# Kernel tuning notes

Hardware: AMD Instinct MI355X
Metric: run time of the kernel (lower is better)

Reference implementation:

```python
import jax, jax.numpy as jnp
import numpy as np

B, R, N, D, H = 32, 5, 1024, 256, 256

def setup_inputs() -> dict:
    key = jax.random.key(0)
    k1, k2, k3, k4 = jax.random.split(key, 4)
    nodes = jax.random.normal(k1, (B, N, D), dtype=jnp.float32)
    adj = jax.random.uniform(k2, (B, R, N, N), dtype=jnp.float32)
    # kaiming_normal_ approximation: std = sqrt(2 / fan_in)
    std = np.sqrt(2.0 / D).astype(np.float32)
    w_0 = jax.random.normal(k3, (H, D), dtype=jnp.float32) * std
    w_r = jax.random.normal(k4, (R, H, D), dtype=jnp.float32) * std
    return {"nodes": nodes, "adj": adj, "w_0": w_0, "w_r": w_r}

def reference(nodes, adj, w_0, w_r):
    # nodes: (B,N,D), adj: (B,R,N,N), w_0: (H,D), w_r: (R,H,D)
    xw_0 = jnp.einsum('bnd,hd->bnh', nodes, w_0)            # (B,N,H)
    xw_r = jnp.einsum('bnd,rhd->brnh', nodes, w_r)          # (B,R,N,H)
    c_r = jnp.sum(adj, axis=-1, keepdims=True)              # (B,R,N,1)
    c_r = jnp.where(c_r == 0, jnp.ones_like(c_r), c_r)
    out = jnp.sum(xw_r / c_r, axis=1) + xw_0                # (B,N,H)
    # dropout is identity in eval mode
    return out
```

## Files before the change

### kernel.cpp

```cpp
#include <hip/hip_runtime.h>
#include <hip/hip_bf16.h>


#define BB 32
#define RR 5
#define NN 1024
#define DD 256
#define HH 256
#define MM (BB * NN)

typedef __attribute__((ext_vector_type(8))) short short8;
typedef __attribute__((ext_vector_type(4))) float f32x4;

__device__ __forceinline__ unsigned short f2bf(float f) {
    unsigned int u = __float_as_uint(f);
    unsigned int r = (u + 0x7FFFu + ((u >> 16) & 1u)) >> 16;
    return (unsigned short)r;
}

__global__ void cvt_kernel(const float* __restrict__ in,
                           unsigned short* __restrict__ out, int n) {
    int i = (blockIdx.x * blockDim.x + threadIdx.x) * 4;
    if (i >= n) return;
    float4 v = *reinterpret_cast<const float4*>(in + i);
    ushort4 o;
    o.x = f2bf(v.x); o.y = f2bf(v.y); o.z = f2bf(v.z); o.w = f2bf(v.w);
    *reinterpret_cast<ushort4*>(out + i) = o;
}

__global__ __launch_bounds__(256) void rowsum_kernel(const float* __restrict__ adj,
                                                     float* __restrict__ inv_c) {
    const int wave = blockIdx.x * 4 + (threadIdx.x >> 6);
    const int lane = threadIdx.x & 63;
    const float4* row4 = reinterpret_cast<const float4*>(adj + (size_t)wave * NN);
    float s = 0.f;
#pragma unroll
    for (int i = 0; i < 4; ++i) {
        float4 v = row4[lane + 64 * i];
        s += (v.x + v.y) + (v.z + v.w);
    }
#pragma unroll
    for (int off = 32; off > 0; off >>= 1) s += __shfl_down(s, off, 64);
    if (lane == 0) {
        float c = (s == 0.f) ? 1.f : s;
        inv_c[wave] = 1.f / c;
    }
}

__global__ __launch_bounds__(256) void gemm_kernel(
    const unsigned short* __restrict__ nodesb,
    const unsigned short* __restrict__ wb,
    const float* __restrict__ inv_c,
    float* __restrict__ out) {
    const int lane = threadIdx.x & 63;
    const int wv   = threadIdx.x >> 6;
    const int row_base = blockIdx.x * 64;
    const int col_base = blockIdx.y * 64 + wv * 16;
    const int m    = lane & 15;
    const int quad = lane >> 4;
    const int kofs = quad * 8;

    f32x4 acc[6][4];
#pragma unroll
    for (int s = 0; s < 6; ++s)
#pragma unroll
        for (int t = 0; t < 4; ++t) acc[s][t] = (f32x4){0.f, 0.f, 0.f, 0.f};

    const unsigned short* aptr = nodesb + (size_t)(row_base + m) * DD + kofs;
    const unsigned short* bptr = wb + (size_t)(col_base + m) * DD + kofs;

#pragma unroll
    for (int k = 0; k < DD; k += 32) {
        short8 afr[4];
#pragma unroll
        for (int t = 0; t < 4; ++t)
            afr[t] = *reinterpret_cast<const short8*>(aptr + (size_t)t * 16 * DD + k);
#pragma unroll
        for (int s = 0; s < 6; ++s) {
            short8 bfr = *reinterpret_cast<const short8*>(bptr + (size_t)s * HH * DD + k);
#pragma unroll
            for (int t = 0; t < 4; ++t)
                acc[s][t] = __builtin_amdgcn_mfma_f32_16x16x32_bf16(afr[t], bfr, acc[s][t], 0, 0, 0);
        }
    }

    const int b  = row_base >> 10;
    const int n0 = row_base & (NN - 1);
#pragma unroll
    for (int t = 0; t < 4; ++t) {
#pragma unroll
        for (int i = 0; i < 4; ++i) {
            const int rloc = t * 16 + quad * 4 + i;
            const int n = n0 + rloc;
            float v = acc[0][t][i];
#pragma unroll
            for (int r = 0; r < RR; ++r)
                v += inv_c[((size_t)b * RR + r) * NN + n] * acc[r + 1][t][i];
            out[((size_t)(row_base + rloc)) * HH + col_base + m] = v;
        }
    }
}

extern "C" void kernel_launch(void* const* d_in, const int* in_sizes, int n_in,
                              void* d_out, int out_size, void* d_ws, size_t ws_size,
                              hipStream_t stream) {
    const float* nodes = (const float*)d_in[0];
    const float* adj   = (const float*)d_in[1];
    const float* w0    = (const float*)d_in[2];
    const float* wr    = (const float*)d_in[3];
    float* out = (float*)d_out;

    unsigned short* nodesb = (unsigned short*)d_ws;
    unsigned short* wb     = (unsigned short*)((char*)d_ws + (size_t)MM * DD * 2);
    float*          inv_c  = (float*)((char*)d_ws + (size_t)MM * DD * 2 + (size_t)6 * HH * DD * 2);

    const int n_nodes = MM * DD;
    const int n_w0    = HH * DD;
    const int n_wr    = RR * HH * DD;

    cvt_kernel<<<n_nodes / 4 / 256, 256, 0, stream>>>(nodes, nodesb, n_nodes);
    cvt_kernel<<<n_w0 / 4 / 256, 256, 0, stream>>>(w0, wb, n_w0);
    cvt_kernel<<<n_wr / 4 / 256, 256, 0, stream>>>(wr, wb + n_w0, n_wr);

    rowsum_kernel<<<(BB * RR * NN) / 4, 256, 0, stream>>>(adj, inv_c);

    gemm_kernel<<<dim3(MM / 64, HH / 64), 256, 0, stream>>>(nodesb, wb, inv_c, out);
}
```

Baseline: 962.9 us.

## Stage GEMM A/B tiles through LDS via direct global-to-LDS loads

New measurement: 906.4 us. 5.9% less time.

```diff
diff --git a/kernel.cpp b/kernel.cpp
--- a/kernel.cpp
+++ b/kernel.cpp
@@ -11,6 +11,9 @@
 
 typedef __attribute__((ext_vector_type(8))) short short8;
 typedef __attribute__((ext_vector_type(4))) float f32x4;
+
+#define GAS(p) ((const __attribute__((address_space(1))) void*)(p))
+#define LAS(p) ((__attribute__((address_space(3))) void*)(p))
 
 __device__ __forceinline__ unsigned short f2bf(float f) {
     unsigned int u = __float_as_uint(f);
@@ -52,13 +55,37 @@
     const unsigned short* __restrict__ wb,
     const float* __restrict__ inv_c,
     float* __restrict__ out) {
-    const int lane = threadIdx.x & 63;
-    const int wv   = threadIdx.x >> 6;
+    __shared__ unsigned short smem[14336];
+    __shared__ float s_inv[RR * 64];
+
+    const int tid  = threadIdx.x;
+    const int lane = tid & 63;
+    const int wv   = tid >> 6;
     const int row_base = blockIdx.x * 64;
-    const int col_base = blockIdx.y * 64 + wv * 16;
+    const int col_base = blockIdx.y * 64;
     const int m    = lane & 15;
     const int quad = lane >> 4;
-    const int kofs = quad * 8;
+
+    const unsigned short* gp[7];
+    unsigned short*       lp[7];
+#pragma unroll
+    for (int j = 0; j < 7; ++j) {
+        const int c = wv * 7 + j;
+        lp[j] = smem + c * 512;
+        if (c < 4) {
+            const int u   = c * 64 + lane;
+            const int row = u >> 2;
+            const int kc  = u & 3;
+            gp[j] = nodesb + (size_t)(row_base + row) * DD + kc * 8;
+        } else {
+            const int u    = (c - 4) * 64 + lane;
+            const int col6 = u >> 2;
+            const int kc   = u & 3;
+            const int set  = col6 >> 6;
+            const int col  = col6 & 63;
+            gp[j] = wb + (size_t)(set * HH + col_base + col) * DD + kc * 8;
+        }
+    }
 
     f32x4 acc[6][4];
 #pragma unroll
@@ -66,18 +93,23 @@
 #pragma unroll
         for (int t = 0; t < 4; ++t) acc[s][t] = (f32x4){0.f, 0.f, 0.f, 0.f};
 
-    const unsigned short* aptr = nodesb + (size_t)(row_base + m) * DD + kofs;
-    const unsigned short* bptr = wb + (size_t)(col_base + m) * DD + kofs;
+    const unsigned short* aL = smem + m * 32 + quad * 8;
+    const unsigned short* bL = smem + 2048 + (wv * 16 + m) * 32 + quad * 8;
 
+    for (int kt = 0; kt < 8; ++kt) {
+        __syncthreads();
 #pragma unroll
-    for (int k = 0; k < DD; k += 32) {
+        for (int j = 0; j < 7; ++j)
+            __builtin_amdgcn_global_load_lds(GAS(gp[j] + kt * 32), LAS(lp[j]), 16, 0, 0);
+        __syncthreads();
+
         short8 afr[4];
 #pragma unroll
         for (int t = 0; t < 4; ++t)
-            afr[t] = *reinterpret_cast<const short8*>(aptr + (size_t)t * 16 * DD + k);
+            afr[t] = *reinterpret_cast<const short8*>(aL + t * 512);
 #pragma unroll
         for (int s = 0; s < 6; ++s) {
-            short8 bfr = *reinterpret_cast<const short8*>(bptr + (size_t)s * HH * DD + k);
+            short8 bfr = *reinterpret_cast<const short8*>(bL + s * 2048);
 #pragma unroll
             for (int t = 0; t < 4; ++t)
                 acc[s][t] = __builtin_amdgcn_mfma_f32_16x16x32_bf16(afr[t], bfr, acc[s][t], 0, 0, 0);
@@ -86,17 +118,25 @@
 
     const int b  = row_base >> 10;
     const int n0 = row_base & (NN - 1);
+    __syncthreads();
+#pragma unroll
+    for (int i = tid; i < RR * 64; i += 256) {
+        const int r = i >> 6, nl = i & 63;
+        s_inv[i] = inv_c[((size_t)b * RR + r) * NN + n0 + nl];
+    }
+    __syncthreads();
+
+    const int hcol = col_base + wv * 16 + m;
 #pragma unroll
     for (int t = 0; t < 4; ++t) {
 #pragma unroll
         for (int i = 0; i < 4; ++i) {
             const int rloc = t * 16 + quad * 4 + i;
-            const int n = n0 + rloc;
             float v = acc[0][t][i];
 #pragma unroll
             for (int r = 0; r < RR; ++r)
-                v += inv_c[((size_t)b * RR + r) * NN + n] * acc[r + 1][t][i];
-            out[((size_t)(row_base + rloc)) * HH + col_base + m] = v;
+                v += s_inv[r * 64 + rloc] * acc[r + 1][t][i];
+            out[(size_t)(row_base + rloc) * HH + hcol] = v;
         }
     }
 }
```
